# Kernel optimization log

Measured on AMD Instinct MI355X. Metric: run time of the kernel, lower is better.

The kernel has to match this reference:

```python
import jax, jax.numpy as jnp
import numpy as np

N_HEADS = 8
DIM = 128
BT, A, M = 2880, 10, 350  # bs*T, agents, map tokens (from forwards())
TOPK_SELF, TOPK_CROSS = 3, 32


def _split_heads(x, h):
    B, T, C = x.shape
    return x.reshape(B, T, h, C // h).transpose(0, 2, 1, 3)  # [B,h,T,hd]


def _biased_attn(q, k, v, pe, rel):
    """flex_attention with score_mod: score + pe[b,q,rel[b,q,kv],h], -inf where rel==-1.
    q:[B,H,Tq,d] k,v:[B,H,Tk,d] pe:[B,Tq,K,H] rel:[B,Tq,Tk] int"""
    d = q.shape[-1]
    scores = jnp.einsum('bhqd,bhkd->bhqk', q, k) / jnp.sqrt(jnp.asarray(d, q.dtype))
    safe = jnp.maximum(rel, 0)
    bias = jnp.take_along_axis(pe, safe[:, :, :, None], axis=2)  # [B,Tq,Tk,H]
    bias = bias.transpose(0, 3, 1, 2)                            # [B,H,Tq,Tk]
    scores = jnp.where(rel[:, None, :, :] > -1, scores + bias, -jnp.inf)
    attn = jax.nn.softmax(scores, axis=-1)
    out = jnp.einsum('bhqk,bhkd->bhqd', attn, v)
    B, H, Tq, hd = out.shape
    return out.transpose(0, 2, 1, 3).reshape(B, Tq, H * hd)


def _make_relation(key, B, Tq, Tk, topk):
    # topk random keys per query get offsets 0..topk-1 in ascending kv order; rest -1
    rand = jax.random.uniform(key, (B, Tq, Tk))
    idx = jnp.sort(jax.lax.top_k(rand, topk)[1], axis=-1)  # [B,Tq,topk]
    rel = jnp.full((B, Tq, Tk), -1, dtype=jnp.int32)
    b = jnp.arange(B)[:, None, None]
    qi = jnp.arange(Tq)[None, :, None]
    return rel.at[b, qi, idx].set(jnp.arange(topk, dtype=jnp.int32)[None, None, :])


def setup_inputs() -> dict:
    key = jax.random.key(0)
    ks = jax.random.split(key, 12)
    s = 0.02
    return {
        'a_token': jax.random.normal(ks[0], (BT, A, DIM), jnp.float32),
        'm_token': jax.random.normal(ks[1], (BT, M, DIM), jnp.float32),
        'a2m_pe': jax.random.uniform(ks[2], (BT, A, TOPK_CROSS, N_HEADS), jnp.float32),
        'a_pe': jax.random.uniform(ks[3], (BT, A, TOPK_SELF, N_HEADS), jnp.float32),
        'Wq': s * jax.random.normal(ks[4], (DIM, DIM), jnp.float32),
        'Wk': s * jax.random.normal(ks[5], (DIM, DIM), jnp.float32),
        'Wv': s * jax.random.normal(ks[6], (DIM, DIM), jnp.float32),
        'W_cross_proj': s * jax.random.normal(ks[7], (DIM, DIM), jnp.float32),
        'W_cattn': s * jax.random.normal(ks[8], (DIM, 3 * DIM), jnp.float32),
        'W_self_proj': s * jax.random.normal(ks[9], (DIM, DIM), jnp.float32),
        'a2m_relation': _make_relation(ks[10], BT, A, M, TOPK_CROSS),
        'a_relation': _make_relation(ks[11], BT, A, A, TOPK_SELF),
    }


def reference(a_token, m_token, a2m_pe, a_pe, Wq, Wk, Wv, W_cross_proj,
              W_cattn, W_self_proj, a2m_relation, a_relation):
    # cross attention: q from a_token, k/v from m_token (dropout=0 => identity)
    q = _split_heads(a_token @ Wq, N_HEADS)
    k = _split_heads(m_token @ Wk, N_HEADS)
    v = _split_heads(m_token @ Wv, N_HEADS)
    y = _biased_attn(q, k, v, a2m_pe, a2m_relation) @ W_cross_proj
    # self attention with fused qkv projection
    q2, k2, v2 = jnp.split(y @ W_cattn, 3, axis=-1)
    y2 = _biased_attn(_split_heads(q2, N_HEADS), _split_heads(k2, N_HEADS),
                      _split_heads(v2, N_HEADS), a_pe, a_relation)
    return y2 @ W_self_proj
```

## Files before the change

### kernel.cpp

```cpp
#include <hip/hip_runtime.h>
#include <hip/hip_bf16.h>


typedef __attribute__((ext_vector_type(4))) float f32x4;
typedef __attribute__((ext_vector_type(8))) short bf16x8v;
typedef __attribute__((ext_vector_type(4))) short short4v;

#define BT_N 2880
#define A_N  10
#define M_N  350
#define BQ_N (BT_N * A_N)
#define DIMC 128

static __device__ __forceinline__ short f2b(float x) {
    __hip_bfloat16 b = __float2bfloat16(x);
    return __builtin_bit_cast(short, b);
}
static __device__ __forceinline__ float b2f(short s) {
    unsigned u = ((unsigned)(unsigned short)s) << 16;
    return __builtin_bit_cast(float, u);
}

__global__ __launch_bounds__(256) void precompute_mats(
    const float* __restrict__ Wq, const float* __restrict__ Wk,
    const float* __restrict__ Wv, const float* __restrict__ Wcp,
    const float* __restrict__ Wc, const float* __restrict__ Wsp,
    short* __restrict__ S1t, short* __restrict__ VP1t,
    short* __restrict__ S2t, short* __restrict__ VP2t)
{
    int gid = blockIdx.x * 256 + threadIdx.x;
    int mat = gid >> 17;
    int idx = gid & 131071;
    float acc = 0.f;
    if (mat == 0) {
        int n = idx >> 7, c = idx & 127;
        int h = n >> 7, d = n & 127;
        #pragma unroll
        for (int t = 0; t < 16; ++t)
            acc += Wq[c * 128 + h * 16 + t] * Wk[d * 128 + h * 16 + t];
        S1t[idx] = f2b(acc * 0.25f);
    } else if (mat == 1) {
        int d = idx >> 10, o = idx & 1023;
        int h = o >> 7, c = o & 127;
        #pragma unroll
        for (int t = 0; t < 16; ++t)
            acc += Wv[c * 128 + h * 16 + t] * Wcp[(h * 16 + t) * 128 + d];
        VP1t[idx] = f2b(acc);
    } else if (mat == 2) {
        int n = idx >> 7, c = idx & 127;
        int h = n >> 7, d = n & 127;
        #pragma unroll
        for (int t = 0; t < 16; ++t)
            acc += Wc[c * 384 + h * 16 + t] * Wc[d * 384 + 128 + h * 16 + t];
        S2t[idx] = f2b(acc * 0.25f);
    } else {
        int d = idx >> 10, o = idx & 1023;
        int h = o >> 7, c = o & 127;
        #pragma unroll
        for (int t = 0; t < 16; ++t)
            acc += Wc[c * 384 + 256 + h * 16 + t] * Wsp[(h * 16 + t) * 128 + d];
        VP2t[idx] = f2b(acc);
    }
}

template<bool AF32, bool CF32>
__global__ __launch_bounds__(256) void gemm_bt(
    const void* __restrict__ Ap, const short* __restrict__ Bt,
    void* __restrict__ Cp, int M, int N, int K)
{
    __shared__ short As[128][72];
    __shared__ short Bs[128][72];
    const int tid  = threadIdx.x;
    const int bm   = blockIdx.y << 7, bn = blockIdx.x << 7;
    const int wave = tid >> 6, lane = tid & 63;
    const int wm   = (wave >> 1) << 6, wn = (wave & 1) << 6;
    const int row16 = lane & 15, kq = (lane >> 4) << 3;
    f32x4 acc[4][4] = {};

    for (int k0 = 0; k0 < K; k0 += 64) {
        if (AF32) {
            const float* A = (const float*)Ap;
            #pragma unroll
            for (int i = 0; i < 8; ++i) {
                int f = (i << 8) + tid;
                int r = f >> 4, c = (f & 15) << 2;
                f32x4 v = *(const f32x4*)(A + (size_t)(bm + r) * K + k0 + c);
                short4v t;
                t.x = f2b(v.x); t.y = f2b(v.y); t.z = f2b(v.z); t.w = f2b(v.w);
                *(short4v*)&As[r][c] = t;
            }
        } else {
            const short* A = (const short*)Ap;
            #pragma unroll
            for (int i = 0; i < 4; ++i) {
                int g = (i << 8) + tid;
                int r = g >> 3, c = (g & 7) << 3;
                *(bf16x8v*)&As[r][c] = *(const bf16x8v*)(A + (size_t)(bm + r) * K + k0 + c);
            }
        }
        #pragma unroll
        for (int i = 0; i < 4; ++i) {
            int g = (i << 8) + tid;
            int r = g >> 3, c = (g & 7) << 3;
            *(bf16x8v*)&Bs[r][c] = *(const bf16x8v*)(Bt + (size_t)(bn + r) * K + k0 + c);
        }
        __syncthreads();
        #pragma unroll
        for (int kk = 0; kk < 64; kk += 32) {
            bf16x8v af[4], bfr[4];
            #pragma unroll
            for (int mi = 0; mi < 4; ++mi)
                af[mi] = *(const bf16x8v*)&As[wm + (mi << 4) + row16][kq + kk];
            #pragma unroll
            for (int ni = 0; ni < 4; ++ni)
                bfr[ni] = *(const bf16x8v*)&Bs[wn + (ni << 4) + row16][kq + kk];
            #pragma unroll
            for (int mi = 0; mi < 4; ++mi)
                #pragma unroll
                for (int ni = 0; ni < 4; ++ni)
                    acc[mi][ni] = __builtin_amdgcn_mfma_f32_16x16x32_bf16(
                        af[mi], bfr[ni], acc[mi][ni], 0, 0, 0);
        }
        __syncthreads();
    }

    const int col = lane & 15, rb = (lane >> 4) << 2;
    #pragma unroll
    for (int mi = 0; mi < 4; ++mi)
        #pragma unroll
        for (int ni = 0; ni < 4; ++ni)
            #pragma unroll
            for (int r = 0; r < 4; ++r) {
                int rr = bm + wm + (mi << 4) + rb + r;
                int cc = bn + wn + (ni << 4) + col;
                float v = acc[mi][ni][r];
                if (CF32) ((float*)Cp)[(size_t)rr * N + cc] = v;
                else      ((short*)Cp)[(size_t)rr * N + cc] = f2b(v);
            }
}

__global__ __launch_bounds__(256) void attn_cross(
    const float* __restrict__ m_token, const short* __restrict__ qS,
    const float* __restrict__ pe, const int* __restrict__ rel,
    short* __restrict__ u)
{
    __shared__ float mrows[32][132];
    __shared__ float qsr[1024];
    __shared__ int   selk[32];
    __shared__ float wts[8][32];
    const int bq = blockIdx.x;
    const int b  = bq / A_N;
    const int tid = threadIdx.x;

    const int* relrow = rel + (size_t)bq * M_N;
    for (int k = tid; k < M_N; k += 256) {
        int r = relrow[k];
        if (r >= 0) selk[r] = k;
    }
    {
        short4v v = ((const short4v*)(qS + (size_t)bq * 1024))[tid];
        qsr[(tid << 2) + 0] = b2f(v.x);
        qsr[(tid << 2) + 1] = b2f(v.y);
        qsr[(tid << 2) + 2] = b2f(v.z);
        qsr[(tid << 2) + 3] = b2f(v.w);
    }
    __syncthreads();
    #pragma unroll
    for (int i = 0; i < 4; ++i) {
        int f = (i << 8) + tid;
        int r = f >> 5, c = (f & 31) << 2;
        f32x4 v = *(const f32x4*)(m_token + ((size_t)b * M_N + selk[r]) * DIMC + c);
        *(f32x4*)&mrows[r][c] = v;
    }
    __syncthreads();
    {
        const int h = tid >> 5, r = tid & 31;
        const float* qh = qsr + (h << 7);
        f32x4 p = {0.f, 0.f, 0.f, 0.f};
        #pragma unroll
        for (int d = 0; d < DIMC; d += 4)
            p += *(const f32x4*)(qh + d) * *(const f32x4*)&mrows[r][d];
        float sc = p.x + p.y + p.z + p.w + pe[((size_t)bq * 32 + r) * 8 + h];
        float mx = sc;
        #pragma unroll
        for (int off = 16; off; off >>= 1) mx = fmaxf(mx, __shfl_xor(mx, off, 32));
        float e = expf(sc - mx);
        float s = e;
        #pragma unroll
        for (int off = 16; off; off >>= 1) s += __shfl_xor(s, off, 32);
        wts[h][r] = e / s;
    }
    __syncthreads();
    {
        const int h = tid >> 5, d0 = (tid << 2) & 127;
        f32x4 acc = {0.f, 0.f, 0.f, 0.f};
        #pragma unroll
        for (int r = 0; r < 32; ++r)
            acc += wts[h][r] * *(const f32x4*)&mrows[r][d0];
        short4v t;
        t.x = f2b(acc.x); t.y = f2b(acc.y); t.z = f2b(acc.z); t.w = f2b(acc.w);
        *(short4v*)(u + (size_t)bq * 1024 + (tid << 2)) = t;
    }
}

__global__ __launch_bounds__(256) void attn_self(
    const short* __restrict__ ybf, const short* __restrict__ yS2,
    const float* __restrict__ pe, const int* __restrict__ rel,
    short* __restrict__ u2)
{
    __shared__ float yrows[3][132];
    __shared__ float ysr[1024];
    __shared__ int   selk[3];
    __shared__ float sw[8][3];
    const int bq = blockIdx.x;
    const int b  = bq / A_N;
    const int tid = threadIdx.x;

    if (tid < A_N) {
        int r = rel[(size_t)bq * A_N + tid];
        if (r >= 0) selk[r] = tid;
    }
    {
        short4v v = ((const short4v*)(yS2 + (size_t)bq * 1024))[tid];
        ysr[(tid << 2) + 0] = b2f(v.x);
        ysr[(tid << 2) + 1] = b2f(v.y);
        ysr[(tid << 2) + 2] = b2f(v.z);
        ysr[(tid << 2) + 3] = b2f(v.w);
    }
    __syncthreads();
    if (tid < 48) {
        int r = tid >> 4, c = (tid & 15) << 3;
        bf16x8v v = *(const bf16x8v*)(ybf + ((size_t)b * A_N + selk[r]) * DIMC + c);
        #pragma unroll
        for (int j = 0; j < 8; ++j) yrows[r][c + j] = b2f(v[j]);
    }
    __syncthreads();
    if (tid < 24) {
        int h = tid / 3, r = tid - h * 3;
        const float* qh = ysr + (h << 7);
        f32x4 p = {0.f, 0.f, 0.f, 0.f};
        #pragma unroll
        for (int d = 0; d < DIMC; d += 4)
            p += *(const f32x4*)(qh + d) * *(const f32x4*)&yrows[r][d];
        sw[h][r] = p.x + p.y + p.z + p.w + pe[((size_t)bq * 3 + r) * 8 + h];
    }
    __syncthreads();
    if (tid < 8) {
        float s0 = sw[tid][0], s1 = sw[tid][1], s2 = sw[tid][2];
        float mx = fmaxf(s0, fmaxf(s1, s2));
        float e0 = expf(s0 - mx), e1 = expf(s1 - mx), e2 = expf(s2 - mx);
        float inv = 1.f / (e0 + e1 + e2);
        sw[tid][0] = e0 * inv; sw[tid][1] = e1 * inv; sw[tid][2] = e2 * inv;
    }
    __syncthreads();
    {
        const int h = tid >> 5, d0 = (tid << 2) & 127;
        f32x4 acc = sw[h][0] * *(const f32x4*)&yrows[0][d0]
                  + sw[h][1] * *(const f32x4*)&yrows[1][d0]
                  + sw[h][2] * *(const f32x4*)&yrows[2][d0];
        short4v t;
        t.x = f2b(acc.x); t.y = f2b(acc.y); t.z = f2b(acc.z); t.w = f2b(acc.w);
        *(short4v*)(u2 + (size_t)bq * 1024 + (tid << 2)) = t;
    }
}

extern "C" void kernel_launch(void* const* d_in, const int* in_sizes, int n_in,
                              void* d_out, int out_size, void* d_ws, size_t ws_size,
                              hipStream_t stream)
{
    const float* a_token = (const float*)d_in[0];
    const float* m_token = (const float*)d_in[1];
    const float* a2m_pe  = (const float*)d_in[2];
    const float* a_pe    = (const float*)d_in[3];
    const float* Wq      = (const float*)d_in[4];
    const float* Wk      = (const float*)d_in[5];
    const float* Wv      = (const float*)d_in[6];
    const float* Wcp     = (const float*)d_in[7];
    const float* Wc      = (const float*)d_in[8];
    const float* Wsp     = (const float*)d_in[9];
    const int*   a2m_rel = (const int*)d_in[10];
    const int*   a_rel   = (const int*)d_in[11];

    char* ws = (char*)d_ws;
    short* S1t  = (short*)(ws + 0);
    short* VP1t = (short*)(ws + 262144);
    short* S2t  = (short*)(ws + 524288);
    short* VP2t = (short*)(ws + 786432);
    short* buf1 = (short*)(ws + 1048576);
    short* buf2 = (short*)(ws + 1048576 + 58982400ull);
    short* ybf  = (short*)(ws + 1048576 + 2ull * 58982400ull);
    float* outp = (float*)d_out;

    precompute_mats<<<dim3(2048), dim3(256), 0, stream>>>(
        Wq, Wk, Wv, Wcp, Wc, Wsp, S1t, VP1t, S2t, VP2t);

    gemm_bt<true, false><<<dim3(8, 225), dim3(256), 0, stream>>>(
        (const void*)a_token, S1t, (void*)buf1, BQ_N, 1024, 128);

    attn_cross<<<dim3(BQ_N), dim3(256), 0, stream>>>(
        m_token, buf1, a2m_pe, a2m_rel, buf2);

    gemm_bt<false, false><<<dim3(1, 225), dim3(256), 0, stream>>>(
        (const void*)buf2, VP1t, (void*)ybf, BQ_N, 128, 1024);

    gemm_bt<false, false><<<dim3(8, 225), dim3(256), 0, stream>>>(
        (const void*)ybf, S2t, (void*)buf1, BQ_N, 1024, 128);

    attn_self<<<dim3(BQ_N), dim3(256), 0, stream>>>(
        ybf, buf1, a_pe, a_rel, buf2);

    gemm_bt<false, true><<<dim3(1, 225), dim3(256), 0, stream>>>(
        (const void*)buf2, VP2t, (void*)outp, BQ_N, 128, 1024);
}
```

Measured before the change: 299.8 us.

## Fuse self-attention stage into one per-batch kernel and remap cross-attn blocks per XCD

Replaces three GEMMs plus the self-attention kernel with a single fused kernel that processes four batch groups (40 rows) per block. It computes the y projection, per-head scores, softmax and output projection with MFMA in LDS. Intermediate round-trips through global memory (ybf, buf1, buf2) and several launches are removed. It also remaps cross-attention block indices so that blocks sharing a batch land on the same XCD, for L2 locality. In exchange, the fused kernel uses large LDS with one block per CU and only 720 blocks, and it recomputes per-head products, so occupancy and parallelism drop.

Result: slower. 370.1 us (+23.4%).

```diff
diff --git a/kernel.cpp b/kernel.cpp
--- a/kernel.cpp
+++ b/kernel.cpp
@@ -107,10 +107,10 @@
         __syncthreads();
         #pragma unroll
         for (int kk = 0; kk < 64; kk += 32) {
-            bf16x8v af[4], bfr[4];
+            bf16x8v afr[4], bfr[4];
             #pragma unroll
             for (int mi = 0; mi < 4; ++mi)
-                af[mi] = *(const bf16x8v*)&As[wm + (mi << 4) + row16][kq + kk];
+                afr[mi] = *(const bf16x8v*)&As[wm + (mi << 4) + row16][kq + kk];
             #pragma unroll
             for (int ni = 0; ni < 4; ++ni)
                 bfr[ni] = *(const bf16x8v*)&Bs[wn + (ni << 4) + row16][kq + kk];
@@ -119,7 +119,7 @@
                 #pragma unroll
                 for (int ni = 0; ni < 4; ++ni)
                     acc[mi][ni] = __builtin_amdgcn_mfma_f32_16x16x32_bf16(
-                        af[mi], bfr[ni], acc[mi][ni], 0, 0, 0);
+                        afr[mi], bfr[ni], acc[mi][ni], 0, 0, 0);
         }
         __syncthreads();
     }
@@ -148,8 +148,12 @@
     __shared__ float qsr[1024];
     __shared__ int   selk[32];
     __shared__ float wts[8][32];
-    const int bq = blockIdx.x;
-    const int b  = bq / A_N;
+    const int phys = blockIdx.x;
+    const int xcd  = phys & 7;
+    const int slot = phys >> 3;
+    const int b    = xcd * 360 + slot / A_N;
+    const int q    = slot % A_N;
+    const int bq   = b * A_N + q;
     const int tid = threadIdx.x;
 
     const int* relrow = rel + (size_t)bq * M_N;
@@ -203,64 +207,234 @@
     }
 }
 
-__global__ __launch_bounds__(256) void attn_self(
-    const short* __restrict__ ybf, const short* __restrict__ yS2,
-    const float* __restrict__ pe, const int* __restrict__ rel,
-    short* __restrict__ u2)
+__global__ __launch_bounds__(256, 1) void self_fused(
+    const short* __restrict__ u_in, const short* __restrict__ VP1t,
+    const short* __restrict__ S2t,  const short* __restrict__ VP2t,
+    const float* __restrict__ pe,   const int* __restrict__ rel,
+    float* __restrict__ outp)
 {
-    __shared__ float yrows[3][132];
-    __shared__ float ysr[1024];
-    __shared__ int   selk[3];
-    __shared__ float sw[8][3];
-    const int bq = blockIdx.x;
-    const int b  = bq / A_N;
-    const int tid = threadIdx.x;
-
-    if (tid < A_N) {
-        int r = rel[(size_t)bq * A_N + tid];
-        if (r >= 0) selk[r] = tid;
-    }
+    __shared__ short yL[48][136];
+    __shared__ short bigS[43520];
+    __shared__ short bsL[128][136];
+    __shared__ char  ureg[13056];
+    __shared__ float peL[960];
+    __shared__ int   selS[120];
+
+    short (*aL)[136]  = (short(*)[136])ureg;
+    short (*wLb)[16]  = (short(*)[16])ureg;
+    int*   relL       = (int*)(ureg + 10240);
+
+    const int tid  = threadIdx.x;
+    const int wave = tid >> 6, lane = tid & 63;
+    const int row16 = lane & 15, kq = (lane >> 4) << 3;
+    const int rb4   = (lane >> 4) << 2;
+    const int b0    = blockIdx.x << 2;
+    const size_t rowbase = (size_t)b0 * A_N;
+
+    f32x4 cy[3][2] = {};
+    for (int kc = 0; kc < 8; ++kc) {
+        const int koff = kc << 7;
+        for (int g = tid; g < 640; g += 256) {
+            int r = g >> 4, c8 = (g & 15) << 3;
+            *(bf16x8v*)&aL[r][c8] =
+                *(const bf16x8v*)(u_in + (rowbase + r) * 1024 + koff + c8);
+        }
+        for (int g = tid; g < 2048; g += 256) {
+            int r = g >> 4, c8 = (g & 15) << 3;
+            *(bf16x8v*)&bsL[r][c8] =
+                *(const bf16x8v*)(VP1t + (size_t)r * 1024 + koff + c8);
+        }
+        __syncthreads();
+        #pragma unroll
+        for (int j = 0; j < 2; ++j) {
+            const int nt = (wave << 1) + j;
+            bf16x8v bfr[4];
+            #pragma unroll
+            for (int ks = 0; ks < 4; ++ks)
+                bfr[ks] = *(const bf16x8v*)&bsL[(nt << 4) + row16][(ks << 5) + kq];
+            #pragma unroll
+            for (int mt = 0; mt < 3; ++mt)
+                #pragma unroll
+                for (int ks = 0; ks < 4; ++ks) {
+                    bf16x8v av = *(const bf16x8v*)&aL[(mt << 4) + row16][(ks << 5) + kq];
+                    cy[mt][j] = __builtin_amdgcn_mfma_f32_16x16x32_bf16(
+                        av, bfr[ks], cy[mt][j], 0, 0, 0);
+                }
+        }
+        __syncthreads();
+    }
+    #pragma unroll
+    for (int mt = 0; mt < 3; ++mt)
+        #pragma unroll
+        for (int j = 0; j < 2; ++j)
+            #pragma unroll
+            for (int r = 0; r < 4; ++r) {
+                int a = (mt << 4) + rb4 + r;
+                if (a < 40) yL[a][((wave << 1) + j) * 16 + row16] = f2b(cy[mt][j][r]);
+            }
+    for (int g = tid; g < 1088; g += 256) ((short*)yL)[5440 + g] = 0;
+    __syncthreads();
+
+    bf16x8v af[3][4];
+    #pragma unroll
+    for (int mt = 0; mt < 3; ++mt)
+        #pragma unroll
+        for (int ks = 0; ks < 4; ++ks)
+            af[mt][ks] = *(const bf16x8v*)&yL[(mt << 4) + row16][(ks << 5) + kq];
+
+    for (int g = tid; g < 400; g += 256) {
+        int v = rel[(size_t)b0 * 100 + g];
+        relL[g] = v;
+        if (v >= 0) {
+            int bb = g / 100, rem = g - bb * 100;
+            int q = rem / 10, k = rem - q * 10;
+            selS[bb * 30 + q * 3 + v] = k;
+        }
+    }
+    for (int g = tid; g < 960; g += 256) peL[g] = pe[(size_t)b0 * 240 + g];
+
+    for (int h = 0; h < 8; ++h) {
+        const int n0 = h << 7;
+        for (int g = tid; g < 2048; g += 256) {
+            int r = g >> 4, c8 = (g & 15) << 3;
+            *(bf16x8v*)&bsL[r][c8] =
+                *(const bf16x8v*)(S2t + (size_t)(n0 + r) * 128 + c8);
+        }
+        __syncthreads();
+        f32x4 cc[3][2] = {};
+        #pragma unroll
+        for (int j = 0; j < 2; ++j) {
+            const int nt = (wave << 1) + j;
+            bf16x8v bfr[4];
+            #pragma unroll
+            for (int ks = 0; ks < 4; ++ks)
+                bfr[ks] = *(const bf16x8v*)&bsL[(nt << 4) + row16][(ks << 5) + kq];
+            #pragma unroll
+            for (int mt = 0; mt < 3; ++mt)
+                #pragma unroll
+                for (int ks = 0; ks < 4; ++ks)
+                    cc[mt][j] = __builtin_amdgcn_mfma_f32_16x16x32_bf16(
+                        af[mt][ks], bfr[ks], cc[mt][j], 0, 0, 0);
+        }
+        #pragma unroll
+        for (int mt = 0; mt < 3; ++mt)
+            #pragma unroll
+            for (int j = 0; j < 2; ++j)
+                #pragma unroll
+                for (int r = 0; r < 4; ++r) {
+                    int a = (mt << 4) + rb4 + r;
+                    if (a < 40) {
+                        int bb = (a * 205) >> 11, q = a - bb * 10;
+                        int d = ((wave << 1) + j) * 16 + row16;
+                        bigS[(bb * 80 + q * 8 + h) * 136 + d] = f2b(cc[mt][j][r]);
+                    }
+                }
+        __syncthreads();
+    }
+
     {
-        short4v v = ((const short4v*)(yS2 + (size_t)bq * 1024))[tid];
-        ysr[(tid << 2) + 0] = b2f(v.x);
-        ysr[(tid << 2) + 1] = b2f(v.y);
-        ysr[(tid << 2) + 2] = b2f(v.z);
-        ysr[(tid << 2) + 3] = b2f(v.w);
+        const int bb = wave;
+        bf16x8v bfy[4];
+        #pragma unroll
+        for (int ks = 0; ks < 4; ++ks)
+            bfy[ks] = *(const bf16x8v*)&yL[bb * 10 + row16][(ks << 5) + kq];
+        f32x4 sa[5] = {};
+        #pragma unroll
+        for (int mt = 0; mt < 5; ++mt)
+            #pragma unroll
+            for (int ks = 0; ks < 4; ++ks) {
+                bf16x8v av = *(const bf16x8v*)
+                    &bigS[(bb * 80 + (mt << 4) + row16) * 136 + (ks << 5) + kq];
+                sa[mt] = __builtin_amdgcn_mfma_f32_16x16x32_bf16(
+                    av, bfy[ks], sa[mt], 0, 0, 0);
+            }
+        const int k = row16;
+        #pragma unroll
+        for (int mt = 0; mt < 5; ++mt)
+            #pragma unroll
+            for (int r = 0; r < 4; ++r) {
+                int rowS = (mt << 4) + rb4 + r;
+                int q = rowS >> 3, hh = rowS & 7;
+                int rv = (k < 10) ? relL[bb * 100 + q * 10 + k] : -1;
+                float bias = (rv >= 0) ? peL[bb * 240 + q * 24 + rv * 8 + hh] : 0.f;
+                float s = (rv >= 0) ? sa[mt][r] + bias : -1e30f;
+                float mx = s;
+                mx = fmaxf(mx, __shfl_xor(mx, 8, 16));
+                mx = fmaxf(mx, __shfl_xor(mx, 4, 16));
+                mx = fmaxf(mx, __shfl_xor(mx, 2, 16));
+                mx = fmaxf(mx, __shfl_xor(mx, 1, 16));
+                float e = (rv >= 0) ? __expf(s - mx) : 0.f;
+                float su = e;
+                su += __shfl_xor(su, 8, 16);
+                su += __shfl_xor(su, 4, 16);
+                su += __shfl_xor(su, 2, 16);
+                su += __shfl_xor(su, 1, 16);
+                wLb[bb * 80 + rowS][k] = f2b(e / su);
+            }
     }
     __syncthreads();
-    if (tid < 48) {
-        int r = tid >> 4, c = (tid & 15) << 3;
-        bf16x8v v = *(const bf16x8v*)(ybf + ((size_t)b * A_N + selk[r]) * DIMC + c);
-        #pragma unroll
-        for (int j = 0; j < 8; ++j) yrows[r][c + j] = b2f(v[j]);
-    }
-    __syncthreads();
-    if (tid < 24) {
-        int h = tid / 3, r = tid - h * 3;
-        const float* qh = ysr + (h << 7);
-        f32x4 p = {0.f, 0.f, 0.f, 0.f};
-        #pragma unroll
-        for (int d = 0; d < DIMC; d += 4)
-            p += *(const f32x4*)(qh + d) * *(const f32x4*)&yrows[r][d];
-        sw[h][r] = p.x + p.y + p.z + p.w + pe[((size_t)bq * 3 + r) * 8 + h];
-    }
-    __syncthreads();
-    if (tid < 8) {
-        float s0 = sw[tid][0], s1 = sw[tid][1], s2 = sw[tid][2];
-        float mx = fmaxf(s0, fmaxf(s1, s2));
-        float e0 = expf(s0 - mx), e1 = expf(s1 - mx), e2 = expf(s2 - mx);
-        float inv = 1.f / (e0 + e1 + e2);
-        sw[tid][0] = e0 * inv; sw[tid][1] = e1 * inv; sw[tid][2] = e2 * inv;
-    }
-    __syncthreads();
-    {
-        const int h = tid >> 5, d0 = (tid << 2) & 127;
-        f32x4 acc = sw[h][0] * *(const f32x4*)&yrows[0][d0]
-                  + sw[h][1] * *(const f32x4*)&yrows[1][d0]
-                  + sw[h][2] * *(const f32x4*)&yrows[2][d0];
-        short4v t;
-        t.x = f2b(acc.x); t.y = f2b(acc.y); t.z = f2b(acc.z); t.w = f2b(acc.w);
-        *(short4v*)(u2 + (size_t)bq * 1024 + (tid << 2)) = t;
+
+    for (int h = 0; h < 8; ++h) {
+        const int n0 = h << 7;
+        for (int g = tid; g < 2048; g += 256) {
+            int r = g >> 4, c8 = (g & 15) << 3;
+            *(bf16x8v*)&bsL[r][c8] =
+                *(const bf16x8v*)(VP2t + (size_t)r * 1024 + n0 + c8);
+        }
+        __syncthreads();
+        f32x4 cc[3][2] = {};
+        #pragma unroll
+        for (int j = 0; j < 2; ++j) {
+            const int nt = (wave << 1) + j;
+            bf16x8v bfr[4];
+            #pragma unroll
+            for (int ks = 0; ks < 4; ++ks)
+                bfr[ks] = *(const bf16x8v*)&bsL[(nt << 4) + row16][(ks << 5) + kq];
+            #pragma unroll
+            for (int mt = 0; mt < 3; ++mt)
+                #pragma unroll
+                for (int ks = 0; ks < 4; ++ks)
+                    cc[mt][j] = __builtin_amdgcn_mfma_f32_16x16x32_bf16(
+                        af[mt][ks], bfr[ks], cc[mt][j], 0, 0, 0);
+        }
+        #pragma unroll
+        for (int mt = 0; mt < 3; ++mt)
+            #pragma unroll
+            for (int j = 0; j < 2; ++j)
+                #pragma unroll
+                for (int r = 0; r < 4; ++r) {
+                    int a = (mt << 4) + rb4 + r;
+                    if (a < 40) {
+                        int dl = ((wave << 1) + j) * 16 + row16;
+                        bigS[a * 1040 + n0 + dl] = f2b(cc[mt][j][r]);
+                    }
+                }
+        __syncthreads();
+    }
+
+    for (int idx = tid; idx < 1280; idx += 256) {
+        int a = idx >> 5, d4 = (idx & 31) << 2;
+        int bb = (a * 205) >> 11, q = a - bb * 10;
+        f32x4 acc = {0.f, 0.f, 0.f, 0.f};
+        #pragma unroll
+        for (int hh = 0; hh < 8; ++hh) {
+            int k0s = selS[bb * 30 + q * 3 + 0];
+            int k1s = selS[bb * 30 + q * 3 + 1];
+            int k2s = selS[bb * 30 + q * 3 + 2];
+            float w0 = b2f(wLb[bb * 80 + q * 8 + hh][k0s]);
+            float w1 = b2f(wLb[bb * 80 + q * 8 + hh][k1s]);
+            float w2 = b2f(wLb[bb * 80 + q * 8 + hh][k2s]);
+            float inv = 1.f / (w0 + w1 + w2);
+            short4v z0 = *(const short4v*)&bigS[(bb * 10 + k0s) * 1040 + (hh << 7) + d4];
+            short4v z1 = *(const short4v*)&bigS[(bb * 10 + k1s) * 1040 + (hh << 7) + d4];
+            short4v z2 = *(const short4v*)&bigS[(bb * 10 + k2s) * 1040 + (hh << 7) + d4];
+            w0 *= inv; w1 *= inv; w2 *= inv;
+            acc.x += w0 * b2f(z0.x) + w1 * b2f(z1.x) + w2 * b2f(z2.x);
+            acc.y += w0 * b2f(z0.y) + w1 * b2f(z1.y) + w2 * b2f(z2.y);
+            acc.z += w0 * b2f(z0.z) + w1 * b2f(z1.z) + w2 * b2f(z2.z);
+            acc.w += w0 * b2f(z0.w) + w1 * b2f(z1.w) + w2 * b2f(z2.w);
+        }
+        *(f32x4*)(outp + (rowbase + a) * 128 + d4) = acc;
     }
 }
 
@@ -288,7 +462,6 @@
     short* VP2t = (short*)(ws + 786432);
     short* buf1 = (short*)(ws + 1048576);
     short* buf2 = (short*)(ws + 1048576 + 58982400ull);
-    short* ybf  = (short*)(ws + 1048576 + 2ull * 58982400ull);
     float* outp = (float*)d_out;
 
     precompute_mats<<<dim3(2048), dim3(256), 0, stream>>>(
@@ -300,15 +473,6 @@
     attn_cross<<<dim3(BQ_N), dim3(256), 0, stream>>>(
         m_token, buf1, a2m_pe, a2m_rel, buf2);
 
-    gemm_bt<false, false><<<dim3(1, 225), dim3(256), 0, stream>>>(
-        (const void*)buf2, VP1t, (void*)ybf, BQ_N, 128, 1024);
-
-    gemm_bt<false, false><<<dim3(8, 225), dim3(256), 0, stream>>>(
-        (const void*)ybf, S2t, (void*)buf1, BQ_N, 1024, 128);
-
-    attn_self<<<dim3(BQ_N), dim3(256), 0, stream>>>(
-        ybf, buf1, a_pe, a_rel, buf2);
-
-    gemm_bt<false, true><<<dim3(1, 225), dim3(256), 0, stream>>>(
-        (const void*)buf2, VP2t, (void*)outp, BQ_N, 128, 1024);
-}
+    self_fused<<<dim3(720), dim3(256), 0, stream>>>(
+        buf2, VP1t, S2t, VP2t, a_pe, a_rel, outp);
+}
```

## Use MFMA in cross attention, remap blocks, and add 64-row GEMM for occupancy

Applied to the files above, without the earlier changes.

Rewrites the cross-attention kernel so the gathered map rows are stored as bf16 and both the QK scores and the weighted V sum run through MFMA instructions instead of scalar fp32 dot products. It also remaps block indices so each XCD-sized group of blocks works on contiguous batches, which should improve cache locality for m_token. The two K=1024, N=128 projection GEMMs switch to a 64-row tile variant that launches twice as many blocks to fill more CUs. Softmax now uses the fast __expf. Casting the gathered rows and weights to bf16 loses some precision.

Result: slower. 383.0 us (+27.7%).

```diff
diff --git a/kernel.cpp b/kernel.cpp
--- a/kernel.cpp
+++ b/kernel.cpp
@@ -107,10 +107,10 @@
         __syncthreads();
         #pragma unroll
         for (int kk = 0; kk < 64; kk += 32) {
-            bf16x8v af[4], bfr[4];
+            bf16x8v afr[4], bfr[4];
             #pragma unroll
             for (int mi = 0; mi < 4; ++mi)
-                af[mi] = *(const bf16x8v*)&As[wm + (mi << 4) + row16][kq + kk];
+                afr[mi] = *(const bf16x8v*)&As[wm + (mi << 4) + row16][kq + kk];
             #pragma unroll
             for (int ni = 0; ni < 4; ++ni)
                 bfr[ni] = *(const bf16x8v*)&Bs[wn + (ni << 4) + row16][kq + kk];
@@ -119,7 +119,7 @@
                 #pragma unroll
                 for (int ni = 0; ni < 4; ++ni)
                     acc[mi][ni] = __builtin_amdgcn_mfma_f32_16x16x32_bf16(
-                        af[mi], bfr[ni], acc[mi][ni], 0, 0, 0);
+                        afr[mi], bfr[ni], acc[mi][ni], 0, 0, 0);
         }
         __syncthreads();
     }
@@ -139,67 +139,164 @@
             }
 }
 
-__global__ __launch_bounds__(256) void attn_cross(
+template<bool CF32>
+__global__ __launch_bounds__(256) void gemm_bt64(
+    const short* __restrict__ Ap, const short* __restrict__ Bt,
+    void* __restrict__ Cp, int M, int N, int K)
+{
+    __shared__ short As[64][72];
+    __shared__ short Bs[128][72];
+    const int tid  = threadIdx.x;
+    const int bm   = blockIdx.y << 6, bn = blockIdx.x << 7;
+    const int wave = tid >> 6, lane = tid & 63;
+    const int wm   = (wave >> 1) << 5, wn = (wave & 1) << 6;
+    const int row16 = lane & 15, kq = (lane >> 4) << 3;
+    f32x4 acc[2][4] = {};
+
+    for (int k0 = 0; k0 < K; k0 += 64) {
+        #pragma unroll
+        for (int i = 0; i < 2; ++i) {
+            int g = (i << 8) + tid;
+            int r = g >> 3, c = (g & 7) << 3;
+            *(bf16x8v*)&As[r][c] = *(const bf16x8v*)(Ap + (size_t)(bm + r) * K + k0 + c);
+        }
+        #pragma unroll
+        for (int i = 0; i < 4; ++i) {
+            int g = (i << 8) + tid;
+            int r = g >> 3, c = (g & 7) << 3;
+            *(bf16x8v*)&Bs[r][c] = *(const bf16x8v*)(Bt + (size_t)(bn + r) * K + k0 + c);
+        }
+        __syncthreads();
+        #pragma unroll
+        for (int kk = 0; kk < 64; kk += 32) {
+            bf16x8v afr[2], bfr[4];
+            #pragma unroll
+            for (int mi = 0; mi < 2; ++mi)
+                afr[mi] = *(const bf16x8v*)&As[wm + (mi << 4) + row16][kq + kk];
+            #pragma unroll
+            for (int ni = 0; ni < 4; ++ni)
+                bfr[ni] = *(const bf16x8v*)&Bs[wn + (ni << 4) + row16][kq + kk];
+            #pragma unroll
+            for (int mi = 0; mi < 2; ++mi)
+                #pragma unroll
+                for (int ni = 0; ni < 4; ++ni)
+                    acc[mi][ni] = __builtin_amdgcn_mfma_f32_16x16x32_bf16(
+                        afr[mi], bfr[ni], acc[mi][ni], 0, 0, 0);
+        }
+        __syncthreads();
+    }
+
+    const int col = lane & 15, rb = (lane >> 4) << 2;
+    #pragma unroll
+    for (int mi = 0; mi < 2; ++mi)
+        #pragma unroll
+        for (int ni = 0; ni < 4; ++ni)
+            #pragma unroll
+            for (int r = 0; r < 4; ++r) {
+                int rr = bm + wm + (mi << 4) + rb + r;
+                int cc = bn + wn + (ni << 4) + col;
+                float v = acc[mi][ni][r];
+                if (CF32) ((float*)Cp)[(size_t)rr * N + cc] = v;
+                else      ((short*)Cp)[(size_t)rr * N + cc] = f2b(v);
+            }
+}
+
+__global__ __launch_bounds__(256) void attn_cross2(
     const float* __restrict__ m_token, const short* __restrict__ qS,
     const float* __restrict__ pe, const int* __restrict__ rel,
     short* __restrict__ u)
 {
-    __shared__ float mrows[32][132];
-    __shared__ float qsr[1024];
+    __shared__ short mr[32][136];
+    __shared__ short mT[128][40];
+    __shared__ short qsr[16][136];
+    __shared__ float sc[2][32][20];
+    __shared__ short wts[16][40];
+    __shared__ float peL[256];
+    __shared__ short uL[8][136];
     __shared__ int   selk[32];
-    __shared__ float wts[8][32];
-    const int bq = blockIdx.x;
-    const int b  = bq / A_N;
-    const int tid = threadIdx.x;
-
-    const int* relrow = rel + (size_t)bq * M_N;
+
+    const int phys = blockIdx.x;
+    const int b    = (phys & 7) * 360 + (phys >> 3) / A_N;
+    const int q    = (phys >> 3) % A_N;
+    const int bq   = b * A_N + q;
+    const int tid  = threadIdx.x;
+    const int wave = tid >> 6, lane = tid & 63;
+    const int row16 = lane & 15, kq4 = (lane >> 4) << 3, rb4 = (lane >> 4) << 2;
+
     for (int k = tid; k < M_N; k += 256) {
-        int r = relrow[k];
+        int r = rel[(size_t)bq * M_N + k];
         if (r >= 0) selk[r] = k;
     }
     {
         short4v v = ((const short4v*)(qS + (size_t)bq * 1024))[tid];
-        qsr[(tid << 2) + 0] = b2f(v.x);
-        qsr[(tid << 2) + 1] = b2f(v.y);
-        qsr[(tid << 2) + 2] = b2f(v.z);
-        qsr[(tid << 2) + 3] = b2f(v.w);
-    }
-    __syncthreads();
+        *(short4v*)&qsr[tid >> 5][(tid & 31) << 2] = v;
+    }
+    for (int g = tid; g < 1088; g += 256) ((short*)qsr)[1088 + g] = 0;
+    peL[tid] = pe[(size_t)bq * 256 + tid];
+    __syncthreads();
+
     #pragma unroll
     for (int i = 0; i < 4; ++i) {
         int f = (i << 8) + tid;
-        int r = f >> 5, c = (f & 31) << 2;
-        f32x4 v = *(const f32x4*)(m_token + ((size_t)b * M_N + selk[r]) * DIMC + c);
-        *(f32x4*)&mrows[r][c] = v;
-    }
-    __syncthreads();
+        int r = f & 31, c0 = (f >> 5) << 2;
+        f32x4 v = *(const f32x4*)(m_token + ((size_t)b * M_N + selk[r]) * DIMC + c0);
+        short4v t;
+        t.x = f2b(v.x); t.y = f2b(v.y); t.z = f2b(v.z); t.w = f2b(v.w);
+        *(short4v*)&mr[r][c0] = t;
+        mT[c0 + 0][r] = t.x; mT[c0 + 1][r] = t.y;
+        mT[c0 + 2][r] = t.z; mT[c0 + 3][r] = t.w;
+    }
+    __syncthreads();
+
+    {
+        const int mtile = wave & 1, khalf = wave >> 1;
+        f32x4 sacc = {0.f, 0.f, 0.f, 0.f};
+        #pragma unroll
+        for (int ks = 0; ks < 2; ++ks) {
+            const int kk = (khalf << 6) + (ks << 5);
+            bf16x8v a = *(const bf16x8v*)&mr[(mtile << 4) + row16][kk + kq4];
+            bf16x8v bb = *(const bf16x8v*)&qsr[row16][kk + kq4];
+            sacc = __builtin_amdgcn_mfma_f32_16x16x32_bf16(a, bb, sacc, 0, 0, 0);
+        }
+        #pragma unroll
+        for (int r = 0; r < 4; ++r)
+            sc[khalf][(mtile << 4) + rb4 + r][row16] = sacc[r];
+    }
+    __syncthreads();
+
     {
         const int h = tid >> 5, r = tid & 31;
-        const float* qh = qsr + (h << 7);
-        f32x4 p = {0.f, 0.f, 0.f, 0.f};
-        #pragma unroll
-        for (int d = 0; d < DIMC; d += 4)
-            p += *(const f32x4*)(qh + d) * *(const f32x4*)&mrows[r][d];
-        float sc = p.x + p.y + p.z + p.w + pe[((size_t)bq * 32 + r) * 8 + h];
-        float mx = sc;
+        float s = sc[0][r][h] + sc[1][r][h] + peL[r * 8 + h];
+        float mx = s;
         #pragma unroll
         for (int off = 16; off; off >>= 1) mx = fmaxf(mx, __shfl_xor(mx, off, 32));
-        float e = expf(sc - mx);
-        float s = e;
-        #pragma unroll
-        for (int off = 16; off; off >>= 1) s += __shfl_xor(s, off, 32);
-        wts[h][r] = e / s;
-    }
-    __syncthreads();
-    {
-        const int h = tid >> 5, d0 = (tid << 2) & 127;
-        f32x4 acc = {0.f, 0.f, 0.f, 0.f};
-        #pragma unroll
-        for (int r = 0; r < 32; ++r)
-            acc += wts[h][r] * *(const f32x4*)&mrows[r][d0];
-        short4v t;
-        t.x = f2b(acc.x); t.y = f2b(acc.y); t.z = f2b(acc.z); t.w = f2b(acc.w);
-        *(short4v*)(u + (size_t)bq * 1024 + (tid << 2)) = t;
+        float e = __expf(s - mx);
+        float su = e;
+        #pragma unroll
+        for (int off = 16; off; off >>= 1) su += __shfl_xor(su, off, 32);
+        wts[h][r] = f2b(e / su);
+    }
+    __syncthreads();
+
+    {
+        bf16x8v aw = *(const bf16x8v*)&wts[row16][kq4];
+        #pragma unroll
+        for (int j = 0; j < 2; ++j) {
+            const int nt = (wave << 1) + j;
+            bf16x8v bm_ = *(const bf16x8v*)&mT[(nt << 4) + row16][kq4];
+            f32x4 cz = {0.f, 0.f, 0.f, 0.f};
+            cz = __builtin_amdgcn_mfma_f32_16x16x32_bf16(aw, bm_, cz, 0, 0, 0);
+            #pragma unroll
+            for (int r = 0; r < 4; ++r) {
+                int hh = rb4 + r;
+                if (hh < 8) uL[hh][(nt << 4) + row16] = f2b(cz[r]);
+            }
+        }
+    }
+    __syncthreads();
+    if (tid < 128) {
+        int h = tid >> 4, c8 = (tid & 15) << 3;
+        *(bf16x8v*)(u + (size_t)bq * 1024 + h * 128 + c8) = *(const bf16x8v*)&uL[h][c8];
     }
 }
 
@@ -212,8 +309,10 @@
     __shared__ float ysr[1024];
     __shared__ int   selk[3];
     __shared__ float sw[8][3];
-    const int bq = blockIdx.x;
-    const int b  = bq / A_N;
+    const int phys = blockIdx.x;
+    const int b    = (phys & 7) * 360 + (phys >> 3) / A_N;
+    const int q    = (phys >> 3) % A_N;
+    const int bq   = b * A_N + q;
     const int tid = threadIdx.x;
 
     if (tid < A_N) {
@@ -248,7 +347,7 @@
     if (tid < 8) {
         float s0 = sw[tid][0], s1 = sw[tid][1], s2 = sw[tid][2];
         float mx = fmaxf(s0, fmaxf(s1, s2));
-        float e0 = expf(s0 - mx), e1 = expf(s1 - mx), e2 = expf(s2 - mx);
+        float e0 = __expf(s0 - mx), e1 = __expf(s1 - mx), e2 = __expf(s2 - mx);
         float inv = 1.f / (e0 + e1 + e2);
         sw[tid][0] = e0 * inv; sw[tid][1] = e1 * inv; sw[tid][2] = e2 * inv;
     }
@@ -297,11 +396,11 @@
     gemm_bt<true, false><<<dim3(8, 225), dim3(256), 0, stream>>>(
         (const void*)a_token, S1t, (void*)buf1, BQ_N, 1024, 128);
 
-    attn_cross<<<dim3(BQ_N), dim3(256), 0, stream>>>(
+    attn_cross2<<<dim3(BQ_N), dim3(256), 0, stream>>>(
         m_token, buf1, a2m_pe, a2m_rel, buf2);
 
-    gemm_bt<false, false><<<dim3(1, 225), dim3(256), 0, stream>>>(
-        (const void*)buf2, VP1t, (void*)ybf, BQ_N, 128, 1024);
+    gemm_bt64<false><<<dim3(1, 450), dim3(256), 0, stream>>>(
+        buf2, VP1t, (void*)ybf, BQ_N, 128, 1024);
 
     gemm_bt<false, false><<<dim3(8, 225), dim3(256), 0, stream>>>(
         (const void*)ybf, S2t, (void*)buf1, BQ_N, 1024, 128);
@@ -309,6 +408,6 @@
     attn_self<<<dim3(BQ_N), dim3(256), 0, stream>>>(
         ybf, buf1, a_pe, a_rel, buf2);
 
-    gemm_bt<false, true><<<dim3(1, 225), dim3(256), 0, stream>>>(
-        (const void*)buf2, VP2t, (void*)outp, BQ_N, 128, 1024);
-}
+    gemm_bt64<true><<<dim3(1, 450), dim3(256), 0, stream>>>(
+        buf2, VP2t, (void*)outp, BQ_N, 128, 1024);
+}
```
